# Performance work log

Hardware: AMD Instinct MI355X
Metric: run time of the kernel (lower is better)

The kernel has to match this reference:

```python
import jax, jax.numpy as jnp
import numpy as np

NUM_HEADS = 8
NS = 27  # 3x3x3 deformable samples per query


def _resize1d(x, axis, new):
    # linear resize along one axis, align_corners=False (matches F.interpolate); identity if size matches
    old = x.shape[axis]
    if old == new:
        return x
    pos = (jnp.arange(new, dtype=jnp.float32) + 0.5) * (old / new) - 0.5
    f = jnp.floor(pos)
    w = pos - f
    i0 = jnp.clip(f, 0, old - 1).astype(jnp.int32)
    i1 = jnp.clip(f + 1, 0, old - 1).astype(jnp.int32)
    shp = [1] * x.ndim
    shp[axis] = new
    w = w.reshape(shp)
    return jnp.take(x, i0, axis=axis) * (1 - w) + jnp.take(x, i1, axis=axis) * w


def _rel_to_abs(x):
    # x: (b, d, h, w, w+NS-1) -> (b, d, h, w, NS) via the pad/reshape shifting trick
    b, d, h, w, c = x.shape
    x = jnp.pad(x, ((0, 0), (0, 0), (0, 0), (0, 0), (0, 1)))
    x = x.reshape(b, d, h, w * (c + 1))
    x = jnp.pad(x, ((0, 0), (0, 0), (0, 0), (0, NS - 1)))
    x = x.reshape(b, d, h, w + 1, NS + w - 1)
    return x[:, :, :, :w, w - 1:]


def _rel_logits_1d(q, rel_k):
    # q: (BH, 1, A, B, C, hd); rel_k: (C+NS-1, hd) -> (BH, A, B, C, NS)
    logits = jnp.einsum('nzxywd,rd->nzxywr', q, rel_k)
    n, z, a, b, c, r = logits.shape
    return _rel_to_abs(logits.reshape(n, z * a, b, c, r))


def _pos_emb(q, rel_depth, rel_height, rel_width, D, H, W):
    # q: (BH, 1, D, H, W, hd) -> (BH, D, H, W, NS)
    rw = _resize1d(rel_width, 0, W + NS - 1)
    rh = _resize1d(rel_height, 0, H + NS - 1)
    rd = _resize1d(rel_depth, 0, D + NS - 1)
    lw = _rel_logits_1d(q, rw)            # (BH, D, H, W, NS)
    qh = jnp.swapaxes(q, 3, 4)            # (BH, 1, D, W, H, hd)
    lh = _rel_logits_1d(qh, rh)           # (BH, D, W, H, NS)
    qd = jnp.swapaxes(qh, 2, 4)           # (BH, 1, H, W, D, hd)
    ld = _rel_logits_1d(qd, rd)           # (BH, H, W, D, NS)
    # trilinear resize of lh/ld to (D, H, W) over spatial axes (identity when D==H==W)
    for ax, tgt in ((1, D), (2, H), (3, W)):
        lh = _resize1d(lh, ax, tgt)
        ld = _resize1d(ld, ax, tgt)
    return lw + lh + ld


def _deform_unfold3d(x, offset):
    # x: (BH, C, D, H, W); offset: (BH, NS*3, D, H, W) -> (BH, C*NS, D*H*W)
    BH, C, D, H, W = x.shape
    off = offset.reshape(BH, NS, 3, D, H, W)
    k = jnp.arange(NS)
    kz = (k // 9 - 1).astype(jnp.float32)
    ky = (k // 3 % 3 - 1).astype(jnp.float32)
    kx = (k % 3 - 1).astype(jnp.float32)
    zz, yy, xx = jnp.meshgrid(jnp.arange(D, dtype=jnp.float32),
                              jnp.arange(H, dtype=jnp.float32),
                              jnp.arange(W, dtype=jnp.float32), indexing='ij')
    pz = zz + kz[:, None, None, None] + off[:, :, 0]   # (BH, NS, D, H, W)
    py = yy + ky[:, None, None, None] + off[:, :, 1]
    px = xx + kx[:, None, None, None] + off[:, :, 2]
    z0 = jnp.floor(pz); y0 = jnp.floor(py); x0 = jnp.floor(px)
    wz = pz - z0; wy = py - y0; wx = px - x0
    z0 = z0.astype(jnp.int32); y0 = y0.astype(jnp.int32); x0 = x0.astype(jnp.int32)
    S = D * H * W
    xf = x.reshape(BH, C, S)
    acc = jnp.zeros((BH, C, NS * S), dtype=x.dtype)
    for dz in (0, 1):
        for dy in (0, 1):
            for dx in (0, 1):
                zi = z0 + dz; yi = y0 + dy; xi = x0 + dx
                valid = ((zi >= 0) & (zi < D) & (yi >= 0) & (yi < H) & (xi >= 0) & (xi < W)).astype(x.dtype)
                w = (wz if dz else 1 - wz) * (wy if dy else 1 - wy) * (wx if dx else 1 - wx) * valid
                idx = (jnp.clip(zi, 0, D - 1) * H + jnp.clip(yi, 0, H - 1)) * W + jnp.clip(xi, 0, W - 1)
                g = jnp.take_along_axis(xf, idx.reshape(BH, 1, NS * S), axis=2)  # (BH, C, NS*S)
                acc = acc + g * w.reshape(BH, 1, NS * S)
    return acc.reshape(BH, C * NS, S)


def _forward(x, w_qkv, w_proj, b_proj, w_off, rel_depth, rel_height, rel_width, D, H, W):
    B, N, C = x.shape
    nh = NUM_HEADS
    hd = C // nh
    scale = hd ** -0.5
    BH = B * nh
    qkv = (x @ w_qkv.T).reshape(B, N, 3, nh, hd)
    q = qkv[:, :, 0].transpose(0, 2, 1, 3)  # (B, nh, N, hd)
    k = qkv[:, :, 1].transpose(0, 2, 1, 3)
    v = qkv[:, :, 2].transpose(0, 2, 1, 3)
    offset = (x.reshape(B, N, nh, hd) @ w_off.T).transpose(0, 2, 3, 1).reshape(BH, NS * 3, D, H, W)
    kmap = k.transpose(0, 1, 3, 2).reshape(BH, hd, D, H, W)
    vmap = v.transpose(0, 1, 3, 2).reshape(BH, hd, D, H, W)
    ks = _deform_unfold3d(kmap, offset).transpose(0, 2, 1).reshape(B, nh, N, hd, NS)
    vs = _deform_unfold3d(vmap, offset).reshape(B, nh, hd, NS, N).transpose(0, 1, 4, 3, 2)  # (B, nh, N, NS, hd)
    attn = jnp.einsum('bhnd,bhnds->bhns', q, ks) * scale
    pos = _pos_emb(q.reshape(BH, 1, D, H, W, hd), rel_depth, rel_height, rel_width, D, H, W).reshape(B, nh, N, NS)
    attn = jax.nn.softmax(attn + pos, axis=-1)
    out = jnp.einsum('bhns,bhnsd->bhnd', attn, vs).transpose(0, 2, 1, 3).reshape(B, N, C)
    return out @ w_proj.T + b_proj


def setup_inputs():
    key = jax.random.key(0)
    ks = jax.random.split(key, 8)
    B, D, H, W, C = 1, 16, 16, 16, 512
    N = D * H * W
    hd = C // NUM_HEADS
    return {
        'x': jax.random.normal(ks[0], (B, N, C), dtype=jnp.float32),
        'w_qkv': jax.random.normal(ks[1], (3 * C, C), dtype=jnp.float32) * 0.02,
        'w_proj': jax.random.normal(ks[2], (C, C), dtype=jnp.float32) * 0.02,
        'b_proj': jnp.zeros((C,), dtype=jnp.float32),
        'w_off': jax.random.normal(ks[3], (NS * 3, hd), dtype=jnp.float32) * 0.01,
        'rel_depth': jax.random.normal(ks[4], (D + NS - 1, hd), dtype=jnp.float32) * hd ** -0.5,
        'rel_height': jax.random.normal(ks[5], (H + NS - 1, hd), dtype=jnp.float32) * hd ** -0.5,
        'rel_width': jax.random.normal(ks[6], (W + NS - 1, hd), dtype=jnp.float32) * hd ** -0.5,
        'D': D, 'H': H, 'W': W,
    }


def reference(x, w_qkv, w_proj, b_proj, w_off, rel_depth, rel_height, rel_width, D, H, W):
    return _forward(x, w_qkv, w_proj, b_proj, w_off, rel_depth, rel_height, rel_width, D, H, W)
```

## Files before the change

### kernel.cpp

```cpp
#include <hip/hip_runtime.h>
#include <hip/hip_fp16.h>
#include <math.h>
#include <stdint.h>

#define NH    8
#define HD    64
#define NTOK  4096
#define CDIM  512
#define NSAMP 27

typedef __attribute__((ext_vector_type(8))) _Float16 half8;
typedef __attribute__((ext_vector_type(4))) float floatx4;
typedef unsigned short ushort_t;

__device__ __forceinline__ ushort_t f16b(float f) {
  return __half_as_ushort(__float2half(f));
}
__device__ __forceinline__ __half2 u2h2(uint32_t u) { return __builtin_bit_cast(__half2, u); }
__device__ __forceinline__ uint32_t h22u(__half2 h) { return __builtin_bit_cast(uint32_t, h); }

__device__ __forceinline__ float wave_sum_bcast(float x) {
#define DPP_STEP(ctrl, rmask)                                                   \
  { int t = __builtin_amdgcn_update_dpp(0, __float_as_int(x), ctrl, rmask, 0xf, \
                                        true);                                  \
    x += __int_as_float(t); }
  DPP_STEP(0x111, 0xf)
  DPP_STEP(0x112, 0xf)
  DPP_STEP(0x114, 0xf)
  DPP_STEP(0x118, 0xf)
  DPP_STEP(0x142, 0xa)
  DPP_STEP(0x143, 0xc)
#undef DPP_STEP
  return __int_as_float(__builtin_amdgcn_readlane(__float_as_int(x), 63));
}

__global__ __launch_bounds__(256) void k_cvt(const float4* __restrict__ x,
                                             const float4* __restrict__ wq,
                                             const float4* __restrict__ wp,
                                             ushort_t* __restrict__ xb,
                                             ushort_t* __restrict__ wqb,
                                             ushort_t* __restrict__ wpb) {
  int i = blockIdx.x * 256 + threadIdx.x;
  const float4* src; ushort_t* dst; int off;
  if (i < 524288)      { src = x;  dst = xb;  off = i; }
  else if (i < 720896) { src = wq; dst = wqb; off = i - 524288; }
  else                 { src = wp; dst = wpb; off = i - 720896; }
  float4 v = src[off];
  ushort4 o = make_ushort4(f16b(v.x), f16b(v.y), f16b(v.z), f16b(v.w));
  *(ushort4*)&dst[(size_t)off * 4] = o;
}

__global__ __launch_bounds__(256) void k_cvt2(const float* __restrict__ w_off,
                                              const float* __restrict__ rel_d,
                                              const float* __restrict__ rel_h,
                                              const float* __restrict__ rel_w,
                                              ushort_t* __restrict__ w_offh,
                                              ushort_t* __restrict__ relh) {
  int i = blockIdx.x * 256 + threadIdx.x;
  int row = (i & 8191) >> 6, d = i & 63;
  if (i < 8192) {
    float v = (row < 81) ? w_off[row * 64 + d] : 0.f;
    w_offh[row * 64 + d] = f16b(v);
  } else {
    float v;
    if (row < 42)       v = rel_w[row * 64 + d];
    else if (row < 84)  v = rel_h[(row - 42) * 64 + d];
    else if (row < 126) v = rel_d[(row - 84) * 64 + d];
    else                v = 0.f;
    relh[row * 64 + d] = f16b(v);
  }
}

__global__ __launch_bounds__(256) void k_qkv(const ushort_t* __restrict__ Ah,
                                             const ushort_t* __restrict__ Bth,
                                             ushort_t* __restrict__ qh16,
                                             uint32_t* __restrict__ kvb) {
  __shared__ __align__(16) ushort_t As[128 * 32];
  __shared__ __align__(16) ushort_t Bs[128 * 32];
  const int tid = threadIdx.x;
  const int wave = tid >> 6, lane = tid & 63;
  const int wr = wave >> 1, wc = wave & 1;
  const int m15 = lane & 15, quad = lane >> 4;
  const int bm = blockIdx.x, bn = blockIdx.y;
  floatx4 acc[4][4];
#pragma unroll
  for (int i = 0; i < 4; i++)
#pragma unroll
    for (int j = 0; j < 4; j++) acc[i][j] = {0.f, 0.f, 0.f, 0.f};

  const int r0 = tid >> 2, c0 = (tid & 3) * 8;
  const int r1 = r0 + 64;
  for (int k0 = 0; k0 < 512; k0 += 32) {
    *(uint4*)&As[r0 * 32 + c0] = *(const uint4*)&Ah[(size_t)(bm * 128 + r0) * 512 + k0 + c0];
    *(uint4*)&As[r1 * 32 + c0] = *(const uint4*)&Ah[(size_t)(bm * 128 + r1) * 512 + k0 + c0];
    *(uint4*)&Bs[r0 * 32 + c0] = *(const uint4*)&Bth[(size_t)(bn * 128 + r0) * 512 + k0 + c0];
    *(uint4*)&Bs[r1 * 32 + c0] = *(const uint4*)&Bth[(size_t)(bn * 128 + r1) * 512 + k0 + c0];
    __syncthreads();
    half8 af[4], bf[4];
#pragma unroll
    for (int i = 0; i < 4; i++)
      af[i] = *(const half8*)&As[(wr * 64 + i * 16 + m15) * 32 + quad * 8];
#pragma unroll
    for (int j = 0; j < 4; j++)
      bf[j] = *(const half8*)&Bs[(wc * 64 + j * 16 + m15) * 32 + quad * 8];
#pragma unroll
    for (int i = 0; i < 4; i++)
#pragma unroll
      for (int j = 0; j < 4; j++)
        acc[i][j] = __builtin_amdgcn_mfma_f32_16x16x32_f16(af[i], bf[j], acc[i][j], 0, 0, 0);
    __syncthreads();
  }

  ushort_t* kvh16 = (ushort_t*)kvb;
#pragma unroll
  for (int i = 0; i < 4; i++)
#pragma unroll
    for (int j = 0; j < 4; j++) {
      int col = bn * 128 + wc * 64 + j * 16 + m15;
      int t = col >> 9;
      int h = (col >> 6) & 7;
      int d = col & 63;
#pragma unroll
      for (int r = 0; r < 4; r++) {
        int row = bm * 128 + wr * 64 + i * 16 + quad * 4 + r;
        size_t idx = ((size_t)h * NTOK + row) * 64 + d;
        float v = acc[i][j][r];
        if (t == 0) qh16[idx] = f16b(v);
        else kvh16[idx * 2 + (t - 1)] = f16b(v);
      }
    }
}

__global__ __launch_bounds__(256) void k_offmm(const ushort_t* __restrict__ xh,
                                               const ushort_t* __restrict__ w_offh,
                                               float* __restrict__ obuf) {
  __shared__ __align__(16) ushort_t As[128 * 32];
  __shared__ __align__(16) ushort_t Bs[128 * 32];
  const int tid = threadIdx.x;
  const int wave = tid >> 6, lane = tid & 63;
  const int wr = wave >> 1, wc = wave & 1;
  const int m15 = lane & 15, quad = lane >> 4;
  const int bm = blockIdx.x, h = blockIdx.y;
  floatx4 acc[4][4];
#pragma unroll
  for (int i = 0; i < 4; i++)
#pragma unroll
    for (int j = 0; j < 4; j++) acc[i][j] = {0.f, 0.f, 0.f, 0.f};

  const int r0 = tid >> 2, c0 = (tid & 3) * 8;
  const int r1 = r0 + 64;
  for (int k0 = 0; k0 < 64; k0 += 32) {
    *(uint4*)&As[r0 * 32 + c0] = *(const uint4*)&xh[(size_t)(bm * 128 + r0) * 512 + h * 64 + k0 + c0];
    *(uint4*)&As[r1 * 32 + c0] = *(const uint4*)&xh[(size_t)(bm * 128 + r1) * 512 + h * 64 + k0 + c0];
    *(uint4*)&Bs[r0 * 32 + c0] = *(const uint4*)&w_offh[(size_t)r0 * 64 + k0 + c0];
    *(uint4*)&Bs[r1 * 32 + c0] = *(const uint4*)&w_offh[(size_t)r1 * 64 + k0 + c0];
    __syncthreads();
    half8 af[4], bf[4];
#pragma unroll
    for (int i = 0; i < 4; i++)
      af[i] = *(const half8*)&As[(wr * 64 + i * 16 + m15) * 32 + quad * 8];
#pragma unroll
    for (int j = 0; j < 4; j++)
      bf[j] = *(const half8*)&Bs[(wc * 64 + j * 16 + m15) * 32 + quad * 8];
#pragma unroll
    for (int i = 0; i < 4; i++)
#pragma unroll
      for (int j = 0; j < 4; j++)
        acc[i][j] = __builtin_amdgcn_mfma_f32_16x16x32_f16(af[i], bf[j], acc[i][j], 0, 0, 0);
    __syncthreads();
  }

#pragma unroll
  for (int i = 0; i < 4; i++)
#pragma unroll
    for (int j = 0; j < 4; j++) {
      int col = wc * 64 + j * 16 + m15;
      if (col < 81) {
#pragma unroll
        for (int r = 0; r < 4; r++) {
          int row = bm * 128 + wr * 64 + i * 16 + quad * 4 + r;
          obuf[((size_t)h * NTOK + row) * 81 + col] = acc[i][j][r];
        }
      }
    }
}

__global__ __launch_bounds__(256) void k_posmm(const ushort_t* __restrict__ qh16,
                                               const ushort_t* __restrict__ relh,
                                               float* __restrict__ Pbuf) {
  __shared__ __align__(16) ushort_t As[128 * 32];
  __shared__ __align__(16) ushort_t Bs[128 * 32];
  const int tid = threadIdx.x;
  const int wave = tid >> 6, lane = tid & 63;
  const int wr = wave >> 1, wc = wave & 1;
  const int m15 = lane & 15, quad = lane >> 4;
  const int bm = blockIdx.x, h = blockIdx.y;
  const ushort_t* Ah = qh16 + (size_t)h * NTOK * 64;
  floatx4 acc[4][4];
#pragma unroll
  for (int i = 0; i < 4; i++)
#pragma unroll
    for (int j = 0; j < 4; j++) acc[i][j] = {0.f, 0.f, 0.f, 0.f};

  const int r0 = tid >> 2, c0 = (tid & 3) * 8;
  const int r1 = r0 + 64;
  for (int k0 = 0; k0 < 64; k0 += 32) {
    *(uint4*)&As[r0 * 32 + c0] = *(const uint4*)&Ah[(size_t)(bm * 128 + r0) * 64 + k0 + c0];
    *(uint4*)&As[r1 * 32 + c0] = *(const uint4*)&Ah[(size_t)(bm * 128 + r1) * 64 + k0 + c0];
    *(uint4*)&Bs[r0 * 32 + c0] = *(const uint4*)&relh[(size_t)r0 * 64 + k0 + c0];
    *(uint4*)&Bs[r1 * 32 + c0] = *(const uint4*)&relh[(size_t)r1 * 64 + k0 + c0];
    __syncthreads();
    half8 af[4], bf[4];
#pragma unroll
    for (int i = 0; i < 4; i++)
      af[i] = *(const half8*)&As[(wr * 64 + i * 16 + m15) * 32 + quad * 8];
#pragma unroll
    for (int j = 0; j < 4; j++)
      bf[j] = *(const half8*)&Bs[(wc * 64 + j * 16 + m15) * 32 + quad * 8];
#pragma unroll
    for (int i = 0; i < 4; i++)
#pragma unroll
      for (int j = 0; j < 4; j++)
        acc[i][j] = __builtin_amdgcn_mfma_f32_16x16x32_f16(af[i], bf[j], acc[i][j], 0, 0, 0);
    __syncthreads();
  }

#pragma unroll
  for (int i = 0; i < 4; i++)
#pragma unroll
    for (int j = 0; j < 4; j++) {
      int col = wc * 64 + j * 16 + m15;
      if (col < 126) {
#pragma unroll
        for (int r = 0; r < 4; r++) {
          int row = bm * 128 + wr * 64 + i * 16 + quad * 4 + r;
          Pbuf[((size_t)h * NTOK + row) * 126 + col] = acc[i][j][r];
        }
      }
    }
}

__global__ __launch_bounds__(256) void k_attn(const ushort_t* __restrict__ qh16,
                                              const uint32_t* __restrict__ kvb,
                                              const float* __restrict__ obuf,
                                              const float* __restrict__ Pbuf,
                                              ushort_t* __restrict__ attb16) {
  __shared__ int      s_off[4][NSAMP][8];
  __shared__ uint32_t s_cwh[4][NSAMP][8];
  __shared__ uint32_t vpair[4][14][64];
  __shared__ uint32_t s_wp[4][14];
  const int bid = blockIdx.x;
  const int h = bid & 7;
  const int wave = threadIdx.x >> 6;
  const int lane = threadIdx.x & 63;
  const int n = (bid >> 3) * 4 + wave;
  const int z = n >> 8, y = (n >> 4) & 15, xq = n & 15;
  const float qd = __half2float(__ushort_as_half(qh16[((size_t)h * NTOK + n) * 64 + lane]));
  const char* kvc = (const char*)(kvb + (size_t)h * NTOK * 64);
  const uint32_t lane4 = (uint32_t)lane * 4u;

  if (lane < NSAMP) {
    const int s = lane;
    const float* op = &obuf[((size_t)h * NTOK + n) * 81 + s * 3];
    float oz = op[0], oy = op[1], ox = op[2];
    float pz = (float)(z + (s / 9) - 1) + oz;
    float py = (float)(y + ((s / 3) % 3) - 1) + oy;
    float px = (float)(xq + (s % 3) - 1) + ox;
    float fz = floorf(pz), fy = floorf(py), fx = floorf(px);
    float wz = pz - fz, wy = py - fy, wx = px - fx;
    int z0 = (int)fz, y0 = (int)fy, x0 = (int)fx;
    int      oarr[8];
    uint32_t warr[8];
#pragma unroll
    for (int c = 0; c < 8; c++) {
      int dz = (c >> 2) & 1, dy = (c >> 1) & 1, dx = c & 1;
      int zi = z0 + dz, yi = y0 + dy, xi = x0 + dx;
      bool valid = (zi >= 0) && (zi < 16) && (yi >= 0) && (yi < 16) && (xi >= 0) && (xi < 16);
      float w = (dz ? wz : 1.f - wz) * (dy ? wy : 1.f - wy) * (dx ? wx : 1.f - wx);
      int zc = min(max(zi, 0), 15), yc = min(max(yi, 0), 15), xc = min(max(xi, 0), 15);
      oarr[c] = ((zc * 16 + yc) * 16 + xc) * 256;
      uint32_t hw = (uint32_t)f16b(valid ? w : 0.f);
      warr[c] = hw | (hw << 16);
    }
    *(int4*)&s_off[wave][s][0]  = make_int4(oarr[0], oarr[1], oarr[2], oarr[3]);
    *(int4*)&s_off[wave][s][4]  = make_int4(oarr[4], oarr[5], oarr[6], oarr[7]);
    *(uint4*)&s_cwh[wave][s][0] = make_uint4(warr[0], warr[1], warr[2], warr[3]);
    *(uint4*)&s_cwh[wave][s][4] = make_uint4(warr[4], warr[5], warr[6], warr[7]);
  }

  float mydot = 0.f;
  uint32_t prev_acc = 0;
#pragma unroll 2
  for (int s = 0; s < NSAMP; s++) {
    int4  o0 = *(const int4*)&s_off[wave][s][0];
    int4  o1 = *(const int4*)&s_off[wave][s][4];
    uint4 c0 = *(const uint4*)&s_cwh[wave][s][0];
    uint4 c1 = *(const uint4*)&s_cwh[wave][s][4];
    __half2 acc2 = u2h2(0u);
    uint32_t p;
#define CORNER(OV, WV)                                                       \
    p = *(const uint32_t*)(kvc + (uint32_t)((uint32_t)OV + lane4));          \
    acc2 = __hfma2(u2h2(WV), u2h2(p), acc2);
    CORNER(o0.x, c0.x) CORNER(o0.y, c0.y) CORNER(o0.z, c0.z) CORNER(o0.w, c0.w)
    CORNER(o1.x, c1.x) CORNER(o1.y, c1.y) CORNER(o1.z, c1.z) CORNER(o1.w, c1.w)
#undef CORNER
    float ak = __half2float(acc2.x);
    float tot = wave_sum_bcast(qd * ak);
    mydot = (lane == s) ? tot : mydot;
    uint32_t au = h22u(acc2);
    if (s & 1)
      vpair[wave][s >> 1][lane] = (prev_acc >> 16) | (au & 0xffff0000u);
    else
      prev_acc = au;
  }
  vpair[wave][13][lane] = prev_acc >> 16;

  float logit = -INFINITY;
  if (lane < NSAMP) {
    int j = 15 + lane - xq;
    int n2 = (z * 16 + xq) * 16 + y;
    int n3 = (xq * 16 + z) * 16 + y;
    float pos = Pbuf[((size_t)h * NTOK + n) * 126 + j]
              + Pbuf[((size_t)h * NTOK + n2) * 126 + 42 + j]
              + Pbuf[((size_t)h * NTOK + n3) * 126 + 84 + j];
    logit = mydot * 0.125f + pos;
  }

  float mx = logit;
#pragma unroll
  for (int off = 32; off >= 1; off >>= 1) mx = fmaxf(mx, __shfl_xor(mx, off, 64));
  float e = __expf(logit - mx);
  float sum = e;
#pragma unroll
  for (int off = 32; off >= 1; off >>= 1) sum += __shfl_xor(sum, off, 64);
  const float wgt = e / sum;
  uint32_t hw = (uint32_t)f16b(wgt);
  uint32_t nw = (uint32_t)__shfl_down((int)hw, 1, 64);
  if ((lane & 1) == 0 && lane < 28)
    s_wp[wave][lane >> 1] = hw | (nw << 16);

  __half2 out2 = u2h2(0u);
#pragma unroll
  for (int p2 = 0; p2 < 14; p2++) {
    __half2 v2 = u2h2(vpair[wave][p2][lane]);
    __half2 w2 = u2h2(s_wp[wave][p2]);
    out2 = __hfma2(w2, v2, out2);
  }
  float out = __half2float(out2.x) + __half2float(out2.y);
  attb16[(size_t)n * 512 + h * 64 + lane] = f16b(out);
}

__global__ __launch_bounds__(256) void k_proj(const ushort_t* __restrict__ Ah,
                                              const ushort_t* __restrict__ Bth,
                                              const float* __restrict__ bias,
                                              float* __restrict__ out) {
  __shared__ __align__(16) ushort_t As[128 * 32];
  __shared__ __align__(16) ushort_t Bs[128 * 32];
  const int tid = threadIdx.x;
  const int wave = tid >> 6, lane = tid & 63;
  const int wr = wave >> 1, wc = wave & 1;
  const int m15 = lane & 15, quad = lane >> 4;
  const int bm = blockIdx.x, bn = blockIdx.y;
  floatx4 acc[4][4];
#pragma unroll
  for (int i = 0; i < 4; i++)
#pragma unroll
    for (int j = 0; j < 4; j++) acc[i][j] = {0.f, 0.f, 0.f, 0.f};

  const int r0 = tid >> 2, c0 = (tid & 3) * 8;
  const int r1 = r0 + 64;
  for (int k0 = 0; k0 < 512; k0 += 32) {
    *(uint4*)&As[r0 * 32 + c0] = *(const uint4*)&Ah[(size_t)(bm * 128 + r0) * 512 + k0 + c0];
    *(uint4*)&As[r1 * 32 + c0] = *(const uint4*)&Ah[(size_t)(bm * 128 + r1) * 512 + k0 + c0];
    *(uint4*)&Bs[r0 * 32 + c0] = *(const uint4*)&Bth[(size_t)(bn * 128 + r0) * 512 + k0 + c0];
    *(uint4*)&Bs[r1 * 32 + c0] = *(const uint4*)&Bth[(size_t)(bn * 128 + r1) * 512 + k0 + c0];
    __syncthreads();
    half8 af[4], bf[4];
#pragma unroll
    for (int i = 0; i < 4; i++)
      af[i] = *(const half8*)&As[(wr * 64 + i * 16 + m15) * 32 + quad * 8];
#pragma unroll
    for (int j = 0; j < 4; j++)
      bf[j] = *(const half8*)&Bs[(wc * 64 + j * 16 + m15) * 32 + quad * 8];
#pragma unroll
    for (int i = 0; i < 4; i++)
#pragma unroll
      for (int j = 0; j < 4; j++)
        acc[i][j] = __builtin_amdgcn_mfma_f32_16x16x32_f16(af[i], bf[j], acc[i][j], 0, 0, 0);
    __syncthreads();
  }

#pragma unroll
  for (int i = 0; i < 4; i++)
#pragma unroll
    for (int j = 0; j < 4; j++) {
      int col = bn * 128 + wc * 64 + j * 16 + m15;
      float b = bias[col];
#pragma unroll
      for (int r = 0; r < 4; r++) {
        int row = bm * 128 + wr * 64 + i * 16 + quad * 4 + r;
        out[(size_t)row * 512 + col] = acc[i][j][r] + b;
      }
    }
}

extern "C" void kernel_launch(void* const* d_in, const int* in_sizes, int n_in,
                              void* d_out, int out_size, void* d_ws, size_t ws_size,
                              hipStream_t stream) {
  const float* x      = (const float*)d_in[0];
  const float* w_qkv  = (const float*)d_in[1];
  const float* w_proj = (const float*)d_in[2];
  const float* b_proj = (const float*)d_in[3];
  const float* w_off  = (const float*)d_in[4];
  const float* rel_d  = (const float*)d_in[5];
  const float* rel_h  = (const float*)d_in[6];
  const float* rel_w  = (const float*)d_in[7];

  char* ws = (char*)d_ws;
  uint32_t* kvb    = (uint32_t*)ws; ws += (size_t)NH * NTOK * 64 * 4;
  float*    ob     = (float*)ws;    ws += (size_t)NH * NTOK * 81 * 4;
  float*    Pb     = (float*)ws;    ws += (size_t)NH * NTOK * 126 * 4;
  ushort_t* attb16 = (ushort_t*)ws; ws += (size_t)NTOK * CDIM * 2;
  ushort_t* xh     = (ushort_t*)ws; ws += (size_t)NTOK * CDIM * 2;
  ushort_t* wqh    = (ushort_t*)ws; ws += (size_t)3 * CDIM * CDIM * 2;
  ushort_t* wph    = (ushort_t*)ws; ws += (size_t)CDIM * CDIM * 2;
  ushort_t* qh16   = (ushort_t*)ws; ws += (size_t)NH * NTOK * 64 * 2;
  ushort_t* w_offh = (ushort_t*)ws; ws += (size_t)128 * 64 * 2;
  ushort_t* relh   = (ushort_t*)ws; ws += (size_t)128 * 64 * 2;
  float*    out    = (float*)d_out;

  k_cvt  <<<dim3(3072), dim3(256), 0, stream>>>((const float4*)x, (const float4*)w_qkv,
                                                (const float4*)w_proj, xh, wqh, wph);
  k_cvt2 <<<dim3(64),   dim3(256), 0, stream>>>(w_off, rel_d, rel_h, rel_w, w_offh, relh);
  k_qkv  <<<dim3(32, 12), dim3(256), 0, stream>>>(xh, wqh, qh16, kvb);
  k_offmm<<<dim3(32, 8),  dim3(256), 0, stream>>>(xh, w_offh, ob);
  k_posmm<<<dim3(32, 8),  dim3(256), 0, stream>>>(qh16, relh, Pb);
  k_attn <<<dim3(8192),   dim3(256), 0, stream>>>(qh16, kvb, ob, Pb, attb16);
  k_proj <<<dim3(32, 4),  dim3(256), 0, stream>>>(attb16, wph, b_proj, out);
}
```

Measured before the change: 188.5 us.

## Merge conversion and aux matmul kernels, unroll attention sampling loop

Folds k_cvt2 into k_cvt and merges the offset and positional-embedding matmuls into a single k_aux launch selected by blockIdx.y, which cuts the launch count from seven to five. In the attention kernel, the 27-sample loop is fully unrolled, the dot result is placed with v_writelane instead of a select, and corner-offset setup is spread across 54 lanes. The V staging buffer is changed to a per-lane row layout read with vector loads. Risks are higher register pressure from full unrolling and possible LDS bank conflicts in the new vrow layout.

Measured after the change: 190.3 us. Within noise of the previous version (+1.0%).

```diff
diff --git a/kernel.cpp b/kernel.cpp
--- a/kernel.cpp
+++ b/kernel.cpp
@@ -19,7 +19,7 @@
 __device__ __forceinline__ __half2 u2h2(uint32_t u) { return __builtin_bit_cast(__half2, u); }
 __device__ __forceinline__ uint32_t h22u(__half2 h) { return __builtin_bit_cast(uint32_t, h); }
 
-__device__ __forceinline__ float wave_sum_bcast(float x) {
+__device__ __forceinline__ int wave_sum_i(float x) {
 #define DPP_STEP(ctrl, rmask)                                                   \
   { int t = __builtin_amdgcn_update_dpp(0, __float_as_int(x), ctrl, rmask, 0xf, \
                                         true);                                  \
@@ -31,44 +31,48 @@
   DPP_STEP(0x142, 0xa)
   DPP_STEP(0x143, 0xc)
 #undef DPP_STEP
-  return __int_as_float(__builtin_amdgcn_readlane(__float_as_int(x), 63));
-}
-
-__global__ __launch_bounds__(256) void k_cvt(const float4* __restrict__ x,
-                                             const float4* __restrict__ wq,
-                                             const float4* __restrict__ wp,
+  return __builtin_amdgcn_readlane(__float_as_int(x), 63);
+}
+
+__global__ __launch_bounds__(256) void k_cvt(const float* __restrict__ x,
+                                             const float* __restrict__ wq,
+                                             const float* __restrict__ wp,
+                                             const float* __restrict__ w_off,
+                                             const float* __restrict__ rel_d,
+                                             const float* __restrict__ rel_h,
+                                             const float* __restrict__ rel_w,
                                              ushort_t* __restrict__ xb,
                                              ushort_t* __restrict__ wqb,
-                                             ushort_t* __restrict__ wpb) {
+                                             ushort_t* __restrict__ wpb,
+                                             ushort_t* __restrict__ w_offh,
+                                             ushort_t* __restrict__ relh) {
   int i = blockIdx.x * 256 + threadIdx.x;
-  const float4* src; ushort_t* dst; int off;
-  if (i < 524288)      { src = x;  dst = xb;  off = i; }
-  else if (i < 720896) { src = wq; dst = wqb; off = i - 524288; }
-  else                 { src = wp; dst = wpb; off = i - 720896; }
-  float4 v = src[off];
+  const float4* src = nullptr;
+  ushort_t* dst;
+  int off;
+  float4 v = make_float4(0.f, 0.f, 0.f, 0.f);
+  if (i < 524288)      { src = (const float4*)x;  dst = xb;  off = i; }
+  else if (i < 720896) { src = (const float4*)wq; dst = wqb; off = i - 524288; }
+  else if (i < 786432) { src = (const float4*)wp; dst = wpb; off = i - 720896; }
+  else {
+    int t = i - 786432;
+    if (t < 2048) {
+      off = t;
+      int e = t * 4, row = e >> 6;
+      if (row < 81) v = *(const float4*)&w_off[e];
+      dst = w_offh;
+    } else {
+      off = t - 2048;
+      int e = off * 4, row = e >> 6, col = e & 63;
+      if (row < 42)       v = *(const float4*)&rel_w[row * 64 + col];
+      else if (row < 84)  v = *(const float4*)&rel_h[(row - 42) * 64 + col];
+      else if (row < 126) v = *(const float4*)&rel_d[(row - 84) * 64 + col];
+      dst = relh;
+    }
+  }
+  if (src) v = src[off];
   ushort4 o = make_ushort4(f16b(v.x), f16b(v.y), f16b(v.z), f16b(v.w));
   *(ushort4*)&dst[(size_t)off * 4] = o;
-}
-
-__global__ __launch_bounds__(256) void k_cvt2(const float* __restrict__ w_off,
-                                              const float* __restrict__ rel_d,
-                                              const float* __restrict__ rel_h,
-                                              const float* __restrict__ rel_w,
-                                              ushort_t* __restrict__ w_offh,
-                                              ushort_t* __restrict__ relh) {
-  int i = blockIdx.x * 256 + threadIdx.x;
-  int row = (i & 8191) >> 6, d = i & 63;
-  if (i < 8192) {
-    float v = (row < 81) ? w_off[row * 64 + d] : 0.f;
-    w_offh[row * 64 + d] = f16b(v);
-  } else {
-    float v;
-    if (row < 42)       v = rel_w[row * 64 + d];
-    else if (row < 84)  v = rel_h[(row - 42) * 64 + d];
-    else if (row < 126) v = rel_d[(row - 84) * 64 + d];
-    else                v = 0.f;
-    relh[row * 64 + d] = f16b(v);
-  }
 }
 
 __global__ __launch_bounds__(256) void k_qkv(const ushort_t* __restrict__ Ah,
@@ -131,16 +135,27 @@
     }
 }
 
-__global__ __launch_bounds__(256) void k_offmm(const ushort_t* __restrict__ xh,
-                                               const ushort_t* __restrict__ w_offh,
-                                               float* __restrict__ obuf) {
+__global__ __launch_bounds__(256) void k_aux(const ushort_t* __restrict__ xh,
+                                             const ushort_t* __restrict__ qh16,
+                                             const ushort_t* __restrict__ w_offh,
+                                             const ushort_t* __restrict__ relh,
+                                             float* __restrict__ ob,
+                                             float* __restrict__ Pb) {
   __shared__ __align__(16) ushort_t As[128 * 32];
   __shared__ __align__(16) ushort_t Bs[128 * 32];
   const int tid = threadIdx.x;
   const int wave = tid >> 6, lane = tid & 63;
   const int wr = wave >> 1, wc = wave & 1;
   const int m15 = lane & 15, quad = lane >> 4;
-  const int bm = blockIdx.x, h = blockIdx.y;
+  const int bm = blockIdx.x;
+  const int mode = blockIdx.y >> 3, h = blockIdx.y & 7;
+
+  const ushort_t* A;  int lda;
+  const ushort_t* B;
+  float* C;  int NC;
+  if (mode == 0) { A = xh + h * 64;                 lda = 512; B = w_offh; C = ob + (size_t)h * NTOK * 81;  NC = 81; }
+  else           { A = qh16 + (size_t)h * NTOK * 64; lda = 64;  B = relh;   C = Pb + (size_t)h * NTOK * 126; NC = 126; }
+
   floatx4 acc[4][4];
 #pragma unroll
   for (int i = 0; i < 4; i++)
@@ -150,10 +165,10 @@
   const int r0 = tid >> 2, c0 = (tid & 3) * 8;
   const int r1 = r0 + 64;
   for (int k0 = 0; k0 < 64; k0 += 32) {
-    *(uint4*)&As[r0 * 32 + c0] = *(const uint4*)&xh[(size_t)(bm * 128 + r0) * 512 + h * 64 + k0 + c0];
-    *(uint4*)&As[r1 * 32 + c0] = *(const uint4*)&xh[(size_t)(bm * 128 + r1) * 512 + h * 64 + k0 + c0];
-    *(uint4*)&Bs[r0 * 32 + c0] = *(const uint4*)&w_offh[(size_t)r0 * 64 + k0 + c0];
-    *(uint4*)&Bs[r1 * 32 + c0] = *(const uint4*)&w_offh[(size_t)r1 * 64 + k0 + c0];
+    *(uint4*)&As[r0 * 32 + c0] = *(const uint4*)&A[(size_t)(bm * 128 + r0) * lda + k0 + c0];
+    *(uint4*)&As[r1 * 32 + c0] = *(const uint4*)&A[(size_t)(bm * 128 + r1) * lda + k0 + c0];
+    *(uint4*)&Bs[r0 * 32 + c0] = *(const uint4*)&B[(size_t)r0 * 64 + k0 + c0];
+    *(uint4*)&Bs[r1 * 32 + c0] = *(const uint4*)&B[(size_t)r1 * 64 + k0 + c0];
     __syncthreads();
     half8 af[4], bf[4];
 #pragma unroll
@@ -175,66 +190,11 @@
 #pragma unroll
     for (int j = 0; j < 4; j++) {
       int col = wc * 64 + j * 16 + m15;
-      if (col < 81) {
+      if (col < NC) {
 #pragma unroll
         for (int r = 0; r < 4; r++) {
           int row = bm * 128 + wr * 64 + i * 16 + quad * 4 + r;
-          obuf[((size_t)h * NTOK + row) * 81 + col] = acc[i][j][r];
-        }
-      }
-    }
-}
-
-__global__ __launch_bounds__(256) void k_posmm(const ushort_t* __restrict__ qh16,
-                                               const ushort_t* __restrict__ relh,
-                                               float* __restrict__ Pbuf) {
-  __shared__ __align__(16) ushort_t As[128 * 32];
-  __shared__ __align__(16) ushort_t Bs[128 * 32];
-  const int tid = threadIdx.x;
-  const int wave = tid >> 6, lane = tid & 63;
-  const int wr = wave >> 1, wc = wave & 1;
-  const int m15 = lane & 15, quad = lane >> 4;
-  const int bm = blockIdx.x, h = blockIdx.y;
-  const ushort_t* Ah = qh16 + (size_t)h * NTOK * 64;
-  floatx4 acc[4][4];
-#pragma unroll
-  for (int i = 0; i < 4; i++)
-#pragma unroll
-    for (int j = 0; j < 4; j++) acc[i][j] = {0.f, 0.f, 0.f, 0.f};
-
-  const int r0 = tid >> 2, c0 = (tid & 3) * 8;
-  const int r1 = r0 + 64;
-  for (int k0 = 0; k0 < 64; k0 += 32) {
-    *(uint4*)&As[r0 * 32 + c0] = *(const uint4*)&Ah[(size_t)(bm * 128 + r0) * 64 + k0 + c0];
-    *(uint4*)&As[r1 * 32 + c0] = *(const uint4*)&Ah[(size_t)(bm * 128 + r1) * 64 + k0 + c0];
-    *(uint4*)&Bs[r0 * 32 + c0] = *(const uint4*)&relh[(size_t)r0 * 64 + k0 + c0];
-    *(uint4*)&Bs[r1 * 32 + c0] = *(const uint4*)&relh[(size_t)r1 * 64 + k0 + c0];
-    __syncthreads();
-    half8 af[4], bf[4];
-#pragma unroll
-    for (int i = 0; i < 4; i++)
-      af[i] = *(const half8*)&As[(wr * 64 + i * 16 + m15) * 32 + quad * 8];
-#pragma unroll
-    for (int j = 0; j < 4; j++)
-      bf[j] = *(const half8*)&Bs[(wc * 64 + j * 16 + m15) * 32 + quad * 8];
-#pragma unroll
-    for (int i = 0; i < 4; i++)
-#pragma unroll
-      for (int j = 0; j < 4; j++)
-        acc[i][j] = __builtin_amdgcn_mfma_f32_16x16x32_f16(af[i], bf[j], acc[i][j], 0, 0, 0);
-    __syncthreads();
-  }
-
-#pragma unroll
-  for (int i = 0; i < 4; i++)
-#pragma unroll
-    for (int j = 0; j < 4; j++) {
-      int col = wc * 64 + j * 16 + m15;
-      if (col < 126) {
-#pragma unroll
-        for (int r = 0; r < 4; r++) {
-          int row = bm * 128 + wr * 64 + i * 16 + quad * 4 + r;
-          Pbuf[((size_t)h * NTOK + row) * 126 + col] = acc[i][j][r];
+          C[(size_t)row * NC + col] = acc[i][j][r];
         }
       }
     }
@@ -247,7 +207,7 @@
                                               ushort_t* __restrict__ attb16) {
   __shared__ int      s_off[4][NSAMP][8];
   __shared__ uint32_t s_cwh[4][NSAMP][8];
-  __shared__ uint32_t vpair[4][14][64];
+  __shared__ ushort_t vrow[4][64][28];
   __shared__ uint32_t s_wp[4][14];
   const int bid = blockIdx.x;
   const int h = bid & 7;
@@ -259,8 +219,8 @@
   const char* kvc = (const char*)(kvb + (size_t)h * NTOK * 64);
   const uint32_t lane4 = (uint32_t)lane * 4u;
 
-  if (lane < NSAMP) {
-    const int s = lane;
+  if (lane < 54) {
+    const int s = lane >> 1, half = lane & 1;
     const float* op = &obuf[((size_t)h * NTOK + n) * 81 + s * 3];
     float oz = op[0], oy = op[1], ox = op[2];
     float pz = (float)(z + (s / 9) - 1) + oz;
@@ -269,51 +229,51 @@
     float fz = floorf(pz), fy = floorf(py), fx = floorf(px);
     float wz = pz - fz, wy = py - fy, wx = px - fx;
     int z0 = (int)fz, y0 = (int)fy, x0 = (int)fx;
-    int      oarr[8];
-    uint32_t warr[8];
-#pragma unroll
-    for (int c = 0; c < 8; c++) {
+    int      oarr[4];
+    uint32_t warr[4];
+#pragma unroll
+    for (int cc = 0; cc < 4; cc++) {
+      int c = half * 4 + cc;
       int dz = (c >> 2) & 1, dy = (c >> 1) & 1, dx = c & 1;
       int zi = z0 + dz, yi = y0 + dy, xi = x0 + dx;
       bool valid = (zi >= 0) && (zi < 16) && (yi >= 0) && (yi < 16) && (xi >= 0) && (xi < 16);
       float w = (dz ? wz : 1.f - wz) * (dy ? wy : 1.f - wy) * (dx ? wx : 1.f - wx);
       int zc = min(max(zi, 0), 15), yc = min(max(yi, 0), 15), xc = min(max(xi, 0), 15);
-      oarr[c] = ((zc * 16 + yc) * 16 + xc) * 256;
+      oarr[cc] = ((zc * 16 + yc) * 16 + xc) * 256;
       uint32_t hw = (uint32_t)f16b(valid ? w : 0.f);
-      warr[c] = hw | (hw << 16);
-    }
-    *(int4*)&s_off[wave][s][0]  = make_int4(oarr[0], oarr[1], oarr[2], oarr[3]);
-    *(int4*)&s_off[wave][s][4]  = make_int4(oarr[4], oarr[5], oarr[6], oarr[7]);
-    *(uint4*)&s_cwh[wave][s][0] = make_uint4(warr[0], warr[1], warr[2], warr[3]);
-    *(uint4*)&s_cwh[wave][s][4] = make_uint4(warr[4], warr[5], warr[6], warr[7]);
-  }
-
-  float mydot = 0.f;
-  uint32_t prev_acc = 0;
-#pragma unroll 2
-  for (int s = 0; s < NSAMP; s++) {
-    int4  o0 = *(const int4*)&s_off[wave][s][0];
-    int4  o1 = *(const int4*)&s_off[wave][s][4];
-    uint4 c0 = *(const uint4*)&s_cwh[wave][s][0];
-    uint4 c1 = *(const uint4*)&s_cwh[wave][s][4];
-    __half2 acc2 = u2h2(0u);
-    uint32_t p;
+      warr[cc] = hw | (hw << 16);
+    }
+    *(int4*)&s_off[wave][s][half * 4]  = make_int4(oarr[0], oarr[1], oarr[2], oarr[3]);
+    *(uint4*)&s_cwh[wave][s][half * 4] = make_uint4(warr[0], warr[1], warr[2], warr[3]);
+  }
+  vrow[wave][lane][27] = 0;
+
+  int mydot_i = 0;
 #define CORNER(OV, WV)                                                       \
     p = *(const uint32_t*)(kvc + (uint32_t)((uint32_t)OV + lane4));          \
     acc2 = __hfma2(u2h2(WV), u2h2(p), acc2);
-    CORNER(o0.x, c0.x) CORNER(o0.y, c0.y) CORNER(o0.z, c0.z) CORNER(o0.w, c0.w)
-    CORNER(o1.x, c1.x) CORNER(o1.y, c1.y) CORNER(o1.z, c1.z) CORNER(o1.w, c1.w)
+#define SAMPLE(S)                                                            \
+  {                                                                          \
+    int4  o0 = *(const int4*)&s_off[wave][S][0];                             \
+    int4  o1 = *(const int4*)&s_off[wave][S][4];                             \
+    uint4 c0 = *(const uint4*)&s_cwh[wave][S][0];                            \
+    uint4 c1 = *(const uint4*)&s_cwh[wave][S][4];                            \
+    __half2 acc2 = u2h2(0u);                                                 \
+    uint32_t p;                                                              \
+    CORNER(o0.x, c0.x) CORNER(o0.y, c0.y) CORNER(o0.z, c0.z) CORNER(o0.w, c0.w) \
+    CORNER(o1.x, c1.x) CORNER(o1.y, c1.y) CORNER(o1.z, c1.z) CORNER(o1.w, c1.w) \
+    float ak = __half2float(acc2.x);                                         \
+    int tot_i = wave_sum_i(qd * ak);                                         \
+    asm volatile("v_writelane_b32 %0, %1, %2"                                \
+                 : "+v"(mydot_i) : "s"(tot_i), "i"(S));                      \
+    vrow[wave][lane][S] = (ushort_t)(h22u(acc2) >> 16);                      \
+  }
+  SAMPLE(0)  SAMPLE(1)  SAMPLE(2)  SAMPLE(3)  SAMPLE(4)  SAMPLE(5)  SAMPLE(6)
+  SAMPLE(7)  SAMPLE(8)  SAMPLE(9)  SAMPLE(10) SAMPLE(11) SAMPLE(12) SAMPLE(13)
+  SAMPLE(14) SAMPLE(15) SAMPLE(16) SAMPLE(17) SAMPLE(18) SAMPLE(19) SAMPLE(20)
+  SAMPLE(21) SAMPLE(22) SAMPLE(23) SAMPLE(24) SAMPLE(25) SAMPLE(26)
+#undef SAMPLE
 #undef CORNER
-    float ak = __half2float(acc2.x);
-    float tot = wave_sum_bcast(qd * ak);
-    mydot = (lane == s) ? tot : mydot;
-    uint32_t au = h22u(acc2);
-    if (s & 1)
-      vpair[wave][s >> 1][lane] = (prev_acc >> 16) | (au & 0xffff0000u);
-    else
-      prev_acc = au;
-  }
-  vpair[wave][13][lane] = prev_acc >> 16;
 
   float logit = -INFINITY;
   if (lane < NSAMP) {
@@ -323,7 +283,7 @@
     float pos = Pbuf[((size_t)h * NTOK + n) * 126 + j]
               + Pbuf[((size_t)h * NTOK + n2) * 126 + 42 + j]
               + Pbuf[((size_t)h * NTOK + n3) * 126 + 84 + j];
-    logit = mydot * 0.125f + pos;
+    logit = __int_as_float(mydot_i) * 0.125f + pos;
   }
 
   float mx = logit;
@@ -341,10 +301,10 @@
 
   __half2 out2 = u2h2(0u);
 #pragma unroll
-  for (int p2 = 0; p2 < 14; p2++) {
-    __half2 v2 = u2h2(vpair[wave][p2][lane]);
-    __half2 w2 = u2h2(s_wp[wave][p2]);
-    out2 = __hfma2(w2, v2, out2);
+  for (int p2 = 0; p2 < 7; p2++) {
+    uint2 v2 = *(const uint2*)&vrow[wave][lane][p2 * 4];
+    out2 = __hfma2(u2h2(s_wp[wave][2 * p2]),     u2h2(v2.x), out2);
+    out2 = __hfma2(u2h2(s_wp[wave][2 * p2 + 1]), u2h2(v2.y), out2);
   }
   float out = __half2float(out2.x) + __half2float(out2.y);
   attb16[(size_t)n * 512 + h * 64 + lane] = f16b(out);
@@ -429,12 +389,10 @@
   ushort_t* relh   = (ushort_t*)ws; ws += (size_t)128 * 64 * 2;
   float*    out    = (float*)d_out;
 
-  k_cvt  <<<dim3(3072), dim3(256), 0, stream>>>((const float4*)x, (const float4*)w_qkv,
-                                                (const float4*)w_proj, xh, wqh, wph);
-  k_cvt2 <<<dim3(64),   dim3(256), 0, stream>>>(w_off, rel_d, rel_h, rel_w, w_offh, relh);
-  k_qkv  <<<dim3(32, 12), dim3(256), 0, stream>>>(xh, wqh, qh16, kvb);
-  k_offmm<<<dim3(32, 8),  dim3(256), 0, stream>>>(xh, w_offh, ob);
-  k_posmm<<<dim3(32, 8),  dim3(256), 0, stream>>>(qh16, relh, Pb);
-  k_attn <<<dim3(8192),   dim3(256), 0, stream>>>(qh16, kvb, ob, Pb, attb16);
-  k_proj <<<dim3(32, 4),  dim3(256), 0, stream>>>(attb16, wph, b_proj, out);
-}
+  k_cvt <<<dim3(3088), dim3(256), 0, stream>>>(x, w_qkv, w_proj, w_off, rel_d, rel_h,
+                                               rel_w, xh, wqh, wph, w_offh, relh);
+  k_qkv <<<dim3(32, 12), dim3(256), 0, stream>>>(xh, wqh, qh16, kvb);
+  k_aux <<<dim3(32, 16), dim3(256), 0, stream>>>(xh, qh16, w_offh, relh, ob, Pb);
+  k_attn<<<dim3(8192),   dim3(256), 0, stream>>>(qh16, kvb, ob, Pb, attb16);
+  k_proj<<<dim3(32, 4),  dim3(256), 0, stream>>>(attb16, wph, b_proj, out);
+}
```
